# Performance work log

Hardware: AMD Instinct MI355X
Metric: run time of the kernel (lower is better)

Reference implementation:

```python
import jax, jax.numpy as jnp
import numpy as np

B, T, V, C, H, HS, L, DFF = 8192, 8, 65, 512, 8, 64, 6, 2048
LN_EPS = 1e-5


def _layernorm(x, g, b):
    mu = jnp.mean(x, axis=-1, keepdims=True)
    var = jnp.mean(jnp.square(x - mu), axis=-1, keepdims=True)
    return (x - mu) * jax.lax.rsqrt(var + LN_EPS) * g + b


def setup_inputs() -> dict:
    key = jax.random.key(0)
    ks = jax.random.split(key, 16)
    s = 0.02
    inp = {
        "idx": jax.random.randint(ks[0], (B, T), 0, V),
        "tok_table": jax.random.normal(ks[1], (V, C), jnp.float32) * s,
        "pos_table": jax.random.normal(ks[2], (T, C), jnp.float32) * s,
        "wq": jax.random.normal(ks[3], (L, H, C, HS), jnp.float32) * s,
        "wk": jax.random.normal(ks[4], (L, H, C, HS), jnp.float32) * s,
        "wv": jax.random.normal(ks[5], (L, H, C, HS), jnp.float32) * s,
        "proj_w": jax.random.normal(ks[6], (L, C, C), jnp.float32) * s,
        "proj_b": jnp.zeros((L, C), jnp.float32),
        "w1": jax.random.normal(ks[7], (L, C, DFF), jnp.float32) * s,
        "b1": jnp.zeros((L, DFF), jnp.float32),
        "w2": jax.random.normal(ks[8], (L, DFF, C), jnp.float32) * s,
        "b2": jnp.zeros((L, C), jnp.float32),
        "ln1_g": jnp.ones((L, C), jnp.float32),
        "ln1_b": jnp.zeros((L, C), jnp.float32),
        "ln2_g": jnp.ones((L, C), jnp.float32),
        "ln2_b": jnp.zeros((L, C), jnp.float32),
        "lm_w": jax.random.normal(ks[9], (C, V), jnp.float32) * s,
        "lm_b": jnp.zeros((V,), jnp.float32),
    }
    return inp


def reference(idx, tok_table, pos_table, wq, wk, wv, proj_w, proj_b,
              w1, b1, w2, b2, ln1_g, ln1_b, ln2_g, ln2_b, lm_w, lm_b):
    idx = idx[:, -T:]
    x = tok_table[idx] + pos_table[None, :T, :]  # [B,T,C]
    mask = jnp.tril(jnp.ones((T, T), bool))
    scale = C ** (-0.5)  # NOTE: original scales by n_embed, not head_size
    for l in range(L):
        q = jnp.einsum('btc,hcd->bhtd', x, wq[l])
        k = jnp.einsum('btc,hcd->bhtd', x, wk[l])
        v = jnp.einsum('btc,hcd->bhtd', x, wv[l])
        att = jnp.einsum('bhtd,bhsd->bhts', q, k) * scale
        att = jnp.where(mask, att, -jnp.inf)
        att = jax.nn.softmax(att, axis=-1)
        o = jnp.einsum('bhts,bhsd->bhtd', att, v)
        o = o.transpose(0, 2, 1, 3).reshape(x.shape[0], T, C)  # concat heads
        o = o @ proj_w[l] + proj_b[l]
        x = _layernorm(x + o, ln1_g[l], ln1_b[l])  # post-norm
        h = jax.nn.relu(x @ w1[l] + b1[l]) @ w2[l] + b2[l]
        x = _layernorm(x + h, ln2_g[l], ln2_b[l])
    logits = x @ lm_w + lm_b  # [B,T,V]
    return logits
```

## Files before the change

kernel.cpp:

```cpp
#include <hip/hip_runtime.h>
#include <hip/hip_bf16.h>
#include <math.h>

#define NTOK  65536
#define CDIM  512
#define NHEAD 8
#define HSZ   64
#define NLAYER 6
#define DFF   2048
#define VOCAB 65

typedef unsigned short u16;
typedef __attribute__((ext_vector_type(8))) __bf16 bf16x8;
typedef __attribute__((ext_vector_type(4))) float f32x4;
typedef __attribute__((ext_vector_type(8))) unsigned short ushort8;

__device__ __forceinline__ float b2f(u16 u) {
    union { unsigned int i; float f; } x; x.i = ((unsigned int)u) << 16; return x.f;
}
__device__ __forceinline__ u16 f2b(float f) {
    union { float f; unsigned int i; } x; x.f = f;
    unsigned int r = x.i + 0x7fffu + ((x.i >> 16) & 1u);
    return (u16)(r >> 16);
}

__device__ __forceinline__ void async16(const u16* g, u16* l) {
    __builtin_amdgcn_global_load_lds(
        (const __attribute__((address_space(1))) void*)g,
        (__attribute__((address_space(3))) void*)l, 16, 0, 0);
}

template<int JB, int IB>
__device__ __forceinline__ void mfma_quad(f32x4 (&acc)[4][8],
                                          const bf16x8 (&af)[4][2],
                                          const bf16x8 (&bf)[4][2])
{
#pragma unroll
    for (int kk = 0; kk < 2; kk++)
#pragma unroll
        for (int j = 0; j < 2; j++)
#pragma unroll
            for (int i = 0; i < 4; i++)
                acc[JB + j][IB + i] = __builtin_amdgcn_mfma_f32_16x16x32_bf16(
                    bf[JB + j][kk], af[i][kk], acc[JB + j][IB + i], 0, 0, 0);
}

template<int EPI>
__global__ __launch_bounds__(512, 2)
void gemm256(const u16* __restrict__ A, const u16* __restrict__ Bt,
             void* Cout, const float* __restrict__ bias,
             const u16* res, int K, int lda, int N, int Nout)
{
    extern __shared__ __attribute__((aligned(16))) u16 lds[];
    const int tid = threadIdx.x;

    const int Nx = gridDim.x;
    const int id = blockIdx.y * Nx + blockIdx.x;
    const int xcd = id & 7;
    const int j0 = id >> 3;
    const int mt = xcd + 8 * (j0 / Nx);
    const int nt = j0 - (j0 / Nx) * Nx;
    const int m0 = mt * 256, n0 = nt * 256;

    const int lane = tid & 63, wvv = tid >> 6;
    const int wvm = wvv >> 2, wvn = wvv & 3;
    const int r16 = lane & 15, quad = lane >> 4;
    const int gk0 = quad ^ (r16 & 7);
    const int g0x8 = gk0 * 8, g1x8 = (gk0 ^ 4) * 8;
    const int arow = wvm * 128 + r16;
    const int brow = wvn * 64 + r16;

    const int srow = tid >> 3;
    const int sg = (tid & 7) ^ (srow & 7);
    const u16* pA = A + (size_t)(m0 + srow) * lda + sg * 8;
    const u16* pB = Bt + (size_t)(n0 + srow) * K + sg * 8;
    u16* const ldst = lds + tid * 8;
    const size_t ldaq = (size_t)64 * lda, ldah = (size_t)128 * lda;
    const size_t kq = (size_t)64 * K, kh = (size_t)128 * K;

    const int nk = K >> 6;

    f32x4 acc[4][8] = {};
    bf16x8 af[4][2], bf[4][2];

#define STAGE_A(c, kt, h) do { \
    async16(pA + ((h) ? ldah : 0) + (size_t)((kt) * 64),        ldst + (c) * 32768 + (h) * 8192); \
    async16(pA + ((h) ? ldah : 0) + ldaq + (size_t)((kt) * 64), ldst + (c) * 32768 + (h) * 8192 + 4096); } while (0)
#define STAGE_B(c, kt, h) do { \
    async16(pB + ((h) ? kh : 0) + (size_t)((kt) * 64),          ldst + (c) * 32768 + 16384 + (h) * 8192); \
    async16(pB + ((h) ? kh : 0) + kq + (size_t)((kt) * 64),     ldst + (c) * 32768 + 16384 + (h) * 8192 + 4096); } while (0)
#define LD_A4(IB0) do { _Pragma("unroll") \
    for (int i = 0; i < 4; i++) { \
        const int ro = cb + (arow + ((IB0) + i) * 16) * 64; \
        af[i][0] = *(const bf16x8*)(const void*)&lds[ro + g0x8]; \
        af[i][1] = *(const bf16x8*)(const void*)&lds[ro + g1x8]; \
    } } while (0)
#define LD_B2(JB0) do { _Pragma("unroll") \
    for (int j = 0; j < 2; j++) { \
        const int ro = cb + 16384 + (brow + ((JB0) + j) * 16) * 64; \
        bf[(JB0) + j][0] = *(const bf16x8*)(const void*)&lds[ro + g0x8]; \
        bf[(JB0) + j][1] = *(const bf16x8*)(const void*)&lds[ro + g1x8]; \
    } } while (0)
#define LGKM0() do { asm volatile("s_waitcnt lgkmcnt(0)" ::: "memory"); \
                     __builtin_amdgcn_sched_barrier(0); } while (0)

    STAGE_A(0, 0, 0); STAGE_A(0, 0, 1);
    STAGE_B(0, 0, 0); STAGE_B(0, 0, 1);
    if (nk > 1) {
        STAGE_B(1, 1, 0); STAGE_B(1, 1, 1);
        asm volatile("s_waitcnt vmcnt(4)" ::: "memory");
    } else {
        asm volatile("s_waitcnt vmcnt(0)" ::: "memory");
    }
    __builtin_amdgcn_s_barrier();

    for (int t = 0; t < nk; ++t) {
        const int c = t & 1;
        const int cb = c * 32768;

        LD_A4(0);
        LD_B2(0);
        if (t + 1 < nk) STAGE_A(c ^ 1, t + 1, 0);
        __builtin_amdgcn_s_barrier();
        LGKM0();
        __builtin_amdgcn_s_setprio(1);
        mfma_quad<0, 0>(acc, af, bf);
        __builtin_amdgcn_s_setprio(0);
        __builtin_amdgcn_s_barrier();

        LD_B2(2);
        if (t + 1 < nk) STAGE_A(c ^ 1, t + 1, 1);
        __builtin_amdgcn_s_barrier();
        LGKM0();
        __builtin_amdgcn_s_setprio(1);
        mfma_quad<2, 0>(acc, af, bf);
        __builtin_amdgcn_s_setprio(0);
        __builtin_amdgcn_s_barrier();

        LD_A4(4);
        if (t + 2 < nk) STAGE_B(c, t + 2, 0);
        __builtin_amdgcn_s_barrier();
        LGKM0();
        __builtin_amdgcn_s_setprio(1);
        mfma_quad<0, 4>(acc, af, bf);
        __builtin_amdgcn_s_setprio(0);
        __builtin_amdgcn_s_barrier();

        if (t + 2 < nk) {
            STAGE_B(c, t + 2, 1);
            asm volatile("s_waitcnt vmcnt(4)" ::: "memory");
        } else {
            asm volatile("s_waitcnt vmcnt(0)" ::: "memory");
        }
        __builtin_amdgcn_s_barrier();
        __builtin_amdgcn_s_setprio(1);
        mfma_quad<2, 4>(acc, af, bf);
        __builtin_amdgcn_s_setprio(0);
        __builtin_amdgcn_s_barrier();
    }
#undef STAGE_A
#undef STAGE_B
#undef LD_A4
#undef LD_B2
#undef LGKM0

#pragma unroll
    for (int i = 0; i < 8; i++) {
        const int row = m0 + wvm * 128 + i * 16 + r16;
#pragma unroll
        for (int j = 0; j < 4; j++) {
            const int colb = n0 + wvn * 64 + j * 16 + quad * 4;
            float v[4];
#pragma unroll
            for (int r = 0; r < 4; r++) v[r] = acc[j][i][r];
            if (EPI == 1 || EPI == 2) {
                const f32x4 b4 = *(const f32x4*)(const void*)&bias[colb];
#pragma unroll
                for (int r = 0; r < 4; r++) v[r] += b4[r];
            }
            if (EPI == 1) {
                const uint2 rv = *(const uint2*)(const void*)&res[(size_t)row * N + colb];
                v[0] += b2f((u16)(rv.x & 0xffffu));
                v[1] += b2f((u16)(rv.x >> 16));
                v[2] += b2f((u16)(rv.y & 0xffffu));
                v[3] += b2f((u16)(rv.y >> 16));
            }
            if (EPI == 2) {
#pragma unroll
                for (int r = 0; r < 4; r++) v[r] = fmaxf(v[r], 0.f);
            }
            uint2 o;
            o.x = (unsigned)f2b(v[0]) | ((unsigned)f2b(v[1]) << 16);
            o.y = (unsigned)f2b(v[2]) | ((unsigned)f2b(v[3]) << 16);
            *(uint2*)(void*)&((u16*)Cout)[(size_t)row * N + colb] = o;
        }
    }
}

template<int EPI>
__global__ __launch_bounds__(512)
void gemm_bt(const u16* __restrict__ A, const u16* __restrict__ Bt,
             void* __restrict__ Cout, const float* __restrict__ bias,
             const u16* __restrict__ res, int K, int lda, int N, int Nout)
{
    __shared__ u16 lA[2 * 256 * 32];
    __shared__ u16 lB[2 * 128 * 32];
    const int tid  = threadIdx.x;

    const int Nx = gridDim.x;
    const int id = blockIdx.y * Nx + blockIdx.x;
    const int xcd = id & 7;
    const int j0  = id >> 3;
    const int mt  = xcd + 8 * (j0 / Nx);
    const int nt  = j0 - (j0 / Nx) * Nx;
    const int m0  = mt * 256;
    const int n0  = nt * 128;

    const int lane = tid & 63;
    const int wv   = tid >> 6;
    const int wr   = (wv >> 1) * 64;
    const int wc   = (wv & 1) * 64;
    const int r16  = lane & 15;
    const int quad = lane >> 4;

    f32x4 acc[4][4] = {};

    const int srow = tid >> 2, skseg = (tid & 3) * 8;
    const u16* pA  = A  + (size_t)(m0 + srow) * lda + skseg;
    const u16* pA2 = pA + (size_t)128 * lda;
    const u16* pB  = Bt + (size_t)(n0 + srow) * K + skseg;
    u16* lAt = &lA[(size_t)tid * 8];
    u16* lBt = &lB[(size_t)tid * 8];

    for (int k0 = 0; k0 < K; k0 += 64) {
        async16(pA  + k0,      lAt);
        async16(pA2 + k0,      lAt + 4096);
        async16(pA  + k0 + 32, lAt + 8192);
        async16(pA2 + k0 + 32, lAt + 12288);
        async16(pB  + k0,      lBt);
        async16(pB  + k0 + 32, lBt + 4096);
        __syncthreads();

#pragma unroll
        for (int s = 0; s < 2; s++) {
            const u16* bA = &lA[s * 8192];
            const u16* bB = &lB[s * 4096];
            bf16x8 af[4], bfr[4];
#pragma unroll
            for (int i = 0; i < 4; i++)
                af[i] = *(const bf16x8*)(const void*)&bA[(wr + i * 16 + r16) * 32 + quad * 8];
#pragma unroll
            for (int j = 0; j < 4; j++)
                bfr[j] = *(const bf16x8*)(const void*)&bB[(wc + j * 16 + r16) * 32 + quad * 8];
#pragma unroll
            for (int j = 0; j < 4; j++)
#pragma unroll
                for (int i = 0; i < 4; i++)
                    acc[j][i] = __builtin_amdgcn_mfma_f32_16x16x32_bf16(bfr[j], af[i], acc[j][i], 0, 0, 0);
        }
        __syncthreads();
    }

#pragma unroll
    for (int i = 0; i < 4; i++) {
        const int row = m0 + wr + i * 16 + r16;
#pragma unroll
        for (int j = 0; j < 4; j++) {
            const int colb = n0 + wc + j * 16 + quad * 4;
            float v[4];
#pragma unroll
            for (int r = 0; r < 4; r++) v[r] = acc[j][i][r];
            if (EPI == 3) {
#pragma unroll
                for (int r = 0; r < 4; r++) {
                    const int col = colb + r;
                    if (col < Nout)
                        ((float*)Cout)[(size_t)row * Nout + col] = v[r] + bias[col];
                }
            } else {
                uint2 o;
                o.x = (unsigned)f2b(v[0]) | ((unsigned)f2b(v[1]) << 16);
                o.y = (unsigned)f2b(v[2]) | ((unsigned)f2b(v[3]) << 16);
                *(uint2*)(void*)&((u16*)Cout)[(size_t)row * N + colb] = o;
            }
        }
    }
}

__global__ __launch_bounds__(256)
void attn_k(u16* __restrict__ qkv)
{
    __shared__ float sq[4][8][65], sk[4][8][65], sv[4][8][65], sp[4][64];
    const int w = threadIdx.x >> 6, lane = threadIdx.x & 63;
    const int unit = blockIdx.x * 4 + w;
    const int b = unit >> 3, h = unit & 7;
    const size_t base = (size_t)b * 8 * 1536 + h * 64;
    {
        const int t = lane >> 3, d0 = (lane & 7) * 8;
        const ushort8 q8 = *(const ushort8*)(const void*)&qkv[base + t * 1536 + d0];
        const ushort8 k8 = *(const ushort8*)(const void*)&qkv[base + t * 1536 + 512 + d0];
        const ushort8 v8 = *(const ushort8*)(const void*)&qkv[base + t * 1536 + 1024 + d0];
#pragma unroll
        for (int i = 0; i < 8; i++) {
            sq[w][t][d0 + i] = b2f(q8[i]);
            sk[w][t][d0 + i] = b2f(k8[i]);
            sv[w][t][d0 + i] = b2f(v8[i]);
        }
    }
    __syncthreads();
    const int t = lane >> 3, s = lane & 7;
    float sc = -1e30f;
    if (s <= t) {
        float d = 0.f;
#pragma unroll
        for (int c = 0; c < 64; c++) d += sq[w][t][c] * sk[w][s][c];
        sc = d * 0.04419417382415922f;
    }
    float mx = sc;
#pragma unroll
    for (int m = 1; m < 8; m <<= 1) mx = fmaxf(mx, __shfl_xor(mx, m, 8));
    float e = __expf(sc - mx);
    if (s > t) e = 0.f;
    float sum = e;
#pragma unroll
    for (int m = 1; m < 8; m <<= 1) sum += __shfl_xor(sum, m, 8);
    sp[w][lane] = e / sum;
    __syncthreads();
    {
        const int tt = lane >> 3, d0 = (lane & 7) * 8;
        float a[8] = {};
#pragma unroll
        for (int ss = 0; ss < 8; ss++) {
            const float p = sp[w][tt * 8 + ss];
#pragma unroll
            for (int i = 0; i < 8; i++) a[i] += p * sv[w][ss][d0 + i];
        }
        ushort8 o;
#pragma unroll
        for (int i = 0; i < 8; i++) o[i] = f2b(a[i]);
        *(ushort8*)(void*)&qkv[base + tt * 1536 + d0] = o;
    }
}

__global__ __launch_bounds__(256)
void ln_k(const u16* __restrict__ y, const float* __restrict__ g,
          const float* __restrict__ be, u16* __restrict__ x)
{
    const int w = threadIdx.x >> 6, lane = threadIdx.x & 63;
    const size_t tok = (size_t)blockIdx.x * 4 + w;
    const u16* row = y + tok * 512 + lane * 8;
    ushort8 raw = *(const ushort8*)(const void*)row;
    float v[8];
#pragma unroll
    for (int i = 0; i < 8; i++) v[i] = b2f(raw[i]);
    float s = 0.f;
#pragma unroll
    for (int i = 0; i < 8; i++) s += v[i];
#pragma unroll
    for (int m = 1; m < 64; m <<= 1) s += __shfl_xor(s, m, 64);
    const float mu = s * (1.f / 512.f);
    float q = 0.f;
#pragma unroll
    for (int i = 0; i < 8; i++) { float d = v[i] - mu; q += d * d; }
#pragma unroll
    for (int m = 1; m < 64; m <<= 1) q += __shfl_xor(q, m, 64);
    const float inv = rsqrtf(q * (1.f / 512.f) + 1e-5f);
    f32x4 g0  = *(const f32x4*)(const void*)&g[lane * 8];
    f32x4 g1  = *(const f32x4*)(const void*)&g[lane * 8 + 4];
    f32x4 b0  = *(const f32x4*)(const void*)&be[lane * 8];
    f32x4 b1v = *(const f32x4*)(const void*)&be[lane * 8 + 4];
    ushort8 o;
#pragma unroll
    for (int i = 0; i < 4; i++) o[i]     = f2b((v[i] - mu) * inv * g0[i] + b0[i]);
#pragma unroll
    for (int i = 0; i < 4; i++) o[i + 4] = f2b((v[i + 4] - mu) * inv * g1[i] + b1v[i]);
    *(ushort8*)(void*)&x[tok * 512 + lane * 8] = o;
}

__global__ __launch_bounds__(256)
void embed_k(const int* __restrict__ idx, const float* __restrict__ tokt,
             const float* __restrict__ pos, u16* __restrict__ xb)
{
    const int gid = blockIdx.x * 256 + threadIdx.x;
    const int tk = gid >> 6, seg = (gid & 63) * 8;
    const int t = tk & 7;
    const int ix = idx[tk];
    const f32x4 a0 = *(const f32x4*)(const void*)&tokt[(size_t)ix * 512 + seg];
    const f32x4 a1 = *(const f32x4*)(const void*)&tokt[(size_t)ix * 512 + seg + 4];
    const f32x4 p0 = *(const f32x4*)(const void*)&pos[t * 512 + seg];
    const f32x4 p1 = *(const f32x4*)(const void*)&pos[t * 512 + seg + 4];
    ushort8 o;
#pragma unroll
    for (int i = 0; i < 4; i++) o[i]     = f2b(a0[i] + p0[i]);
#pragma unroll
    for (int i = 0; i < 4; i++) o[i + 4] = f2b(a1[i] + p1[i]);
    *(ushort8*)(void*)&xb[(size_t)tk * 512 + seg] = o;
}

__global__ __launch_bounds__(256)
void conv_t2_k(const float* __restrict__ in, u16* __restrict__ out, int K, int N)
{
    __shared__ float t[32][33];
    const int tx = threadIdx.x & 31, ty4 = (threadIdx.x >> 5) * 4;
    const int n0 = blockIdx.x * 32, k0 = blockIdx.y * 32, l = blockIdx.z;
    const size_t per = (size_t)K * N;
    const float* src = in + l * per;
#pragma unroll
    for (int r = 0; r < 4; r++)
        t[ty4 + r][tx] = src[(size_t)(k0 + ty4 + r) * N + n0 + tx];
    __syncthreads();
    u16* dst = out + l * per;
#pragma unroll
    for (int r = 0; r < 4; r++)
        dst[(size_t)(n0 + ty4 + r) * K + k0 + tx] = f2b(t[tx][ty4 + r]);
}

__global__ __launch_bounds__(256)
void conv_qkv2_k(const float* __restrict__ wq, const float* __restrict__ wk,
                 const float* __restrict__ wv, u16* __restrict__ out)
{
    __shared__ float t[32][33];
    const int tx = threadIdx.x & 31, ty4 = (threadIdx.x >> 5) * 4;
    const int c0 = blockIdx.x * 32, d0 = blockIdx.y * 32;
    const int z = blockIdx.z;
    const int sel = z / 48, rem = z - sel * 48;
    const int l = rem >> 3, h = rem & 7;
    const float* src = (sel == 0) ? wq : (sel == 1) ? wk : wv;
    const float* sb = src + (((size_t)l * 8 + h) * 512) * 64;
#pragma unroll
    for (int r = 0; r < 4; r++)
        t[ty4 + r][tx] = sb[(size_t)(c0 + ty4 + r) * 64 + d0 + tx];
    __syncthreads();
    u16* dst = out + (size_t)l * 786432 + (size_t)(sel * 512 + h * 64 + d0) * 512;
#pragma unroll
    for (int r = 0; r < 4; r++)
        dst[(size_t)(ty4 + r) * 512 + c0 + tx] = f2b(t[tx][ty4 + r]);
}

__global__ __launch_bounds__(256)
void conv_lm_k(const float* __restrict__ lm_w, u16* __restrict__ out)
{
    int gid = blockIdx.x * 256 + threadIdx.x;
    int n = gid >> 9, c = gid & 511;
    out[gid] = (n < VOCAB) ? f2b(lm_w[(size_t)c * VOCAB + n]) : (u16)0;
}

extern "C" void kernel_launch(void* const* d_in, const int* in_sizes, int n_in,
                              void* d_out, int out_size, void* d_ws, size_t ws_size,
                              hipStream_t stream)
{
    const int*   idx    = (const int*)  d_in[0];
    const float* tokt   = (const float*)d_in[1];
    const float* post   = (const float*)d_in[2];
    const float* wq     = (const float*)d_in[3];
    const float* wk     = (const float*)d_in[4];
    const float* wvp    = (const float*)d_in[5];
    const float* proj_w = (const float*)d_in[6];
    const float* proj_b = (const float*)d_in[7];
    const float* w1     = (const float*)d_in[8];
    const float* b1     = (const float*)d_in[9];
    const float* w2     = (const float*)d_in[10];
    const float* b2     = (const float*)d_in[11];
    const float* ln1_g  = (const float*)d_in[12];
    const float* ln1_b  = (const float*)d_in[13];
    const float* ln2_g  = (const float*)d_in[14];
    const float* ln2_b  = (const float*)d_in[15];
    const float* lm_w   = (const float*)d_in[16];
    const float* lm_b   = (const float*)d_in[17];
    float* out = (float*)d_out;

    static int smem_set = 0;
    if (!smem_set) {
        smem_set = 1;
        hipFuncSetAttribute(reinterpret_cast<const void*>(&gemm256<0>),
                            hipFuncAttributeMaxDynamicSharedMemorySize, 131072);
        hipFuncSetAttribute(reinterpret_cast<const void*>(&gemm256<1>),
                            hipFuncAttributeMaxDynamicSharedMemorySize, 131072);
        hipFuncSetAttribute(reinterpret_cast<const void*>(&gemm256<2>),
                            hipFuncAttributeMaxDynamicSharedMemorySize, 131072);
    }

    char* ws = (char*)d_ws;
    u16* wqkvt = (u16*)(ws + 0);
    u16* wprjt = (u16*)(ws + 9437184);
    u16* ww1t  = (u16*)(ws + 12582912);
    u16* ww2t  = (u16*)(ws + 25165824);
    u16* wlmt  = (u16*)(ws + 37748736);
    u16* xb    = (u16*)(ws + 37879808);
    char* big  = ws + 104988672;

    const size_t fixed_bytes = 104988672ull;
    const size_t avail = (ws_size > fixed_bytes) ? (ws_size - fixed_bytes) : 0;
    int chunk_a = 8192, chunk_m = 8192;
    const int cands[3] = {65536, 32768, 16384};
    for (int i = 0; i < 3; i++)
        if ((size_t)cands[i] * 3072ull <= avail) { chunk_a = cands[i]; break; }
    for (int i = 0; i < 3; i++)
        if ((size_t)cands[i] * 4096ull <= avail) { chunk_m = cands[i]; break; }
    const int nca = NTOK / chunk_a, ncm = NTOK / chunk_m;
    u16* qkvc = (u16*)big;
    u16* h1c  = (u16*)big;

    conv_qkv2_k<<<dim3(16, 2, 144), 256, 0, stream>>>(wq, wk, wvp, wqkvt);
    conv_t2_k  <<<dim3(16, 16, 6), 256, 0, stream>>>(proj_w, wprjt, 512, 512);
    conv_t2_k  <<<dim3(64, 16, 6), 256, 0, stream>>>(w1, ww1t, 512, 2048);
    conv_t2_k  <<<dim3(16, 64, 6), 256, 0, stream>>>(w2, ww2t, 2048, 512);
    conv_lm_k  <<<128 * 512 / 256, 256, 0, stream>>>(lm_w, wlmt);

    embed_k<<<NTOK * 64 / 256, 256, 0, stream>>>(idx, tokt, post, xb);

    for (int l = 0; l < NLAYER; l++) {
        for (int c = 0; c < nca; c++) {
            const size_t t0 = (size_t)c * chunk_a;
            gemm256<0><<<dim3(6, chunk_a / 256), 512, 131072, stream>>>(
                xb + t0 * 512, wqkvt + (size_t)l * 786432, qkvc,
                nullptr, nullptr, 512, 512, 1536, 1536);
            attn_k<<<chunk_a / 4, 256, 0, stream>>>(qkvc);
            gemm256<1><<<dim3(2, chunk_a / 256), 512, 131072, stream>>>(
                qkvc, wprjt + (size_t)l * 262144, xb + t0 * 512,
                proj_b + l * 512, xb + t0 * 512, 512, 1536, 512, 512);
        }
        ln_k<<<NTOK / 4, 256, 0, stream>>>(xb, ln1_g + l * 512, ln1_b + l * 512, xb);
        for (int c = 0; c < ncm; c++) {
            const size_t t0 = (size_t)c * chunk_m;
            gemm256<2><<<dim3(8, chunk_m / 256), 512, 131072, stream>>>(
                xb + t0 * 512, ww1t + (size_t)l * 1048576, h1c,
                b1 + l * 2048, nullptr, 512, 512, 2048, 2048);
            gemm256<1><<<dim3(2, chunk_m / 256), 512, 131072, stream>>>(
                h1c, ww2t + (size_t)l * 1048576, xb + t0 * 512,
                b2 + l * 512, xb + t0 * 512, 2048, 2048, 512, 512);
        }
        ln_k<<<NTOK / 4, 256, 0, stream>>>(xb, ln2_g + l * 512, ln2_b + l * 512, xb);
    }

    gemm_bt<3><<<dim3(1, 256), 512, 0, stream>>>(
        xb, wlmt, out, lm_b, nullptr, 512, 512, 128, VOCAB);
}
```

Baseline: 4.115 ms.

## Make gemm256 persistent over N tiles so each block reuses its A rows

The 256-wide GEMM now launches a 1D grid of two blocks per M tile. Each block loops over several consecutive N tiles (tpb), and the B prefetch of the next N tile overlaps with the tail of the current K loop. The goal is to keep the A panel cache-hot and cut block launch and pipeline prologue costs. The trade-offs are fewer blocks, which lowers parallelism when chunks are small, and a serialized epilogue between N tiles.

```diff
diff --git a/kernel.cpp b/kernel.cpp
--- a/kernel.cpp
+++ b/kernel.cpp
@@ -49,18 +49,18 @@
 __global__ __launch_bounds__(512, 2)
 void gemm256(const u16* __restrict__ A, const u16* __restrict__ Bt,
              void* Cout, const float* __restrict__ bias,
-             const u16* res, int K, int lda, int N, int Nout)
+             const u16* res, int K, int lda, int N, int tpb)
 {
     extern __shared__ __attribute__((aligned(16))) u16 lds[];
     const int tid = threadIdx.x;
-
-    const int Nx = gridDim.x;
-    const int id = blockIdx.y * Nx + blockIdx.x;
-    const int xcd = id & 7;
-    const int j0 = id >> 3;
-    const int mt = xcd + 8 * (j0 / Nx);
-    const int nt = j0 - (j0 / Nx) * Nx;
-    const int m0 = mt * 256, n0 = nt * 256;
+    const int bid = blockIdx.x;
+
+    const int per_x = gridDim.x >> 4;
+    const int xcd = bid & 7, wblk = bid >> 3;
+    const int mt = xcd * per_x + (wblk >> 1);
+    const int q  = wblk & 1;
+    const int m0 = mt * 256;
+    const int nt0 = q * tpb;
 
     const int lane = tid & 63, wvv = tid >> 6;
     const int wvm = wvv >> 2, wvn = wvv & 3;
@@ -72,23 +72,24 @@
 
     const int srow = tid >> 3;
     const int sg = (tid & 7) ^ (srow & 7);
-    const u16* pA = A + (size_t)(m0 + srow) * lda + sg * 8;
-    const u16* pB = Bt + (size_t)(n0 + srow) * K + sg * 8;
+    const u16* pA  = A  + (size_t)(m0 + srow) * lda + sg * 8;
+    const u16* pB0 = Bt + (size_t)(nt0 * 256 + srow) * K + sg * 8;
     u16* const ldst = lds + tid * 8;
     const size_t ldaq = (size_t)64 * lda, ldah = (size_t)128 * lda;
     const size_t kq = (size_t)64 * K, kh = (size_t)128 * K;
+    const size_t bstride = (size_t)256 * K;
 
     const int nk = K >> 6;
 
-    f32x4 acc[4][8] = {};
+    f32x4 acc[4][8];
     bf16x8 af[4][2], bf[4][2];
 
 #define STAGE_A(c, kt, h) do { \
     async16(pA + ((h) ? ldah : 0) + (size_t)((kt) * 64),        ldst + (c) * 32768 + (h) * 8192); \
     async16(pA + ((h) ? ldah : 0) + ldaq + (size_t)((kt) * 64), ldst + (c) * 32768 + (h) * 8192 + 4096); } while (0)
-#define STAGE_B(c, kt, h) do { \
-    async16(pB + ((h) ? kh : 0) + (size_t)((kt) * 64),          ldst + (c) * 32768 + 16384 + (h) * 8192); \
-    async16(pB + ((h) ? kh : 0) + kq + (size_t)((kt) * 64),     ldst + (c) * 32768 + 16384 + (h) * 8192 + 4096); } while (0)
+#define STAGE_B(c, pb, kt, h) do { \
+    async16((pb) + ((h) ? kh : 0) + (size_t)((kt) * 64),        ldst + (c) * 32768 + 16384 + (h) * 8192); \
+    async16((pb) + ((h) ? kh : 0) + kq + (size_t)((kt) * 64),   ldst + (c) * 32768 + 16384 + (h) * 8192 + 4096); } while (0)
 #define LD_A4(IB0) do { _Pragma("unroll") \
     for (int i = 0; i < 4; i++) { \
         const int ro = cb + (arow + ((IB0) + i) * 16) * 64; \
@@ -105,96 +106,111 @@
                      __builtin_amdgcn_sched_barrier(0); } while (0)
 
     STAGE_A(0, 0, 0); STAGE_A(0, 0, 1);
-    STAGE_B(0, 0, 0); STAGE_B(0, 0, 1);
+    STAGE_B(0, pB0, 0, 0); STAGE_B(0, pB0, 0, 1);
     if (nk > 1) {
-        STAGE_B(1, 1, 0); STAGE_B(1, 1, 1);
+        STAGE_B(1, pB0, 1, 0); STAGE_B(1, pB0, 1, 1);
         asm volatile("s_waitcnt vmcnt(4)" ::: "memory");
     } else {
         asm volatile("s_waitcnt vmcnt(0)" ::: "memory");
     }
     __builtin_amdgcn_s_barrier();
 
-    for (int t = 0; t < nk; ++t) {
-        const int c = t & 1;
-        const int cb = c * 32768;
-
-        LD_A4(0);
-        LD_B2(0);
-        if (t + 1 < nk) STAGE_A(c ^ 1, t + 1, 0);
-        __builtin_amdgcn_s_barrier();
-        LGKM0();
-        __builtin_amdgcn_s_setprio(1);
-        mfma_quad<0, 0>(acc, af, bf);
-        __builtin_amdgcn_s_setprio(0);
-        __builtin_amdgcn_s_barrier();
-
-        LD_B2(2);
-        if (t + 1 < nk) STAGE_A(c ^ 1, t + 1, 1);
-        __builtin_amdgcn_s_barrier();
-        LGKM0();
-        __builtin_amdgcn_s_setprio(1);
-        mfma_quad<2, 0>(acc, af, bf);
-        __builtin_amdgcn_s_setprio(0);
-        __builtin_amdgcn_s_barrier();
-
-        LD_A4(4);
-        if (t + 2 < nk) STAGE_B(c, t + 2, 0);
-        __builtin_amdgcn_s_barrier();
-        LGKM0();
-        __builtin_amdgcn_s_setprio(1);
-        mfma_quad<0, 4>(acc, af, bf);
-        __builtin_amdgcn_s_setprio(0);
-        __builtin_amdgcn_s_barrier();
-
-        if (t + 2 < nk) {
-            STAGE_B(c, t + 2, 1);
-            asm volatile("s_waitcnt vmcnt(4)" ::: "memory");
-        } else {
-            asm volatile("s_waitcnt vmcnt(0)" ::: "memory");
-        }
-        __builtin_amdgcn_s_barrier();
-        __builtin_amdgcn_s_setprio(1);
-        mfma_quad<2, 4>(acc, af, bf);
-        __builtin_amdgcn_s_setprio(0);
-        __builtin_amdgcn_s_barrier();
+    for (int j = 0; j < tpb; ++j) {
+#pragma unroll
+        for (int jj = 0; jj < 4; jj++)
+#pragma unroll
+            for (int ii = 0; ii < 8; ii++)
+                acc[jj][ii] = (f32x4){0.f, 0.f, 0.f, 0.f};
+
+        for (int t = 0; t < nk; ++t) {
+            const int c = t & 1;
+            const int cb = c * 32768;
+            const bool haveA = !((j == tpb - 1) && (t == nk - 1));
+            const int kta = (t + 1 < nk) ? (t + 1) : 0;
+            int t2 = t + 2, j2 = j;
+            if (t2 >= nk) { t2 -= nk; j2++; }
+            const bool haveB = (j2 < tpb);
+            const u16* pB2 = pB0 + (size_t)j2 * bstride;
+
+            LD_A4(0);
+            LD_B2(0);
+            if (haveA) STAGE_A(c ^ 1, kta, 0);
+            __builtin_amdgcn_s_barrier();
+            LGKM0();
+            __builtin_amdgcn_s_setprio(1);
+            mfma_quad<0, 0>(acc, af, bf);
+            __builtin_amdgcn_s_setprio(0);
+            __builtin_amdgcn_s_barrier();
+
+            LD_B2(2);
+            if (haveA) STAGE_A(c ^ 1, kta, 1);
+            __builtin_amdgcn_s_barrier();
+            LGKM0();
+            __builtin_amdgcn_s_setprio(1);
+            mfma_quad<2, 0>(acc, af, bf);
+            __builtin_amdgcn_s_setprio(0);
+            __builtin_amdgcn_s_barrier();
+
+            LD_A4(4);
+            if (haveB) STAGE_B(c, pB2, t2, 0);
+            __builtin_amdgcn_s_barrier();
+            LGKM0();
+            __builtin_amdgcn_s_setprio(1);
+            mfma_quad<0, 4>(acc, af, bf);
+            __builtin_amdgcn_s_setprio(0);
+            __builtin_amdgcn_s_barrier();
+
+            if (haveB) {
+                STAGE_B(c, pB2, t2, 1);
+                asm volatile("s_waitcnt vmcnt(4)" ::: "memory");
+            } else {
+                asm volatile("s_waitcnt vmcnt(0)" ::: "memory");
+            }
+            __builtin_amdgcn_s_barrier();
+            __builtin_amdgcn_s_setprio(1);
+            mfma_quad<2, 4>(acc, af, bf);
+            __builtin_amdgcn_s_setprio(0);
+            __builtin_amdgcn_s_barrier();
+        }
+
+        const int n0 = (nt0 + j) * 256;
+#pragma unroll
+        for (int i = 0; i < 8; i++) {
+            const int row = m0 + wvm * 128 + i * 16 + r16;
+#pragma unroll
+            for (int jc = 0; jc < 4; jc++) {
+                const int colb = n0 + wvn * 64 + jc * 16 + quad * 4;
+                float v[4];
+#pragma unroll
+                for (int r = 0; r < 4; r++) v[r] = acc[jc][i][r];
+                if (EPI == 1 || EPI == 2) {
+                    const f32x4 b4 = *(const f32x4*)(const void*)&bias[colb];
+#pragma unroll
+                    for (int r = 0; r < 4; r++) v[r] += b4[r];
+                }
+                if (EPI == 1) {
+                    const uint2 rv = *(const uint2*)(const void*)&res[(size_t)row * N + colb];
+                    v[0] += b2f((u16)(rv.x & 0xffffu));
+                    v[1] += b2f((u16)(rv.x >> 16));
+                    v[2] += b2f((u16)(rv.y & 0xffffu));
+                    v[3] += b2f((u16)(rv.y >> 16));
+                }
+                if (EPI == 2) {
+#pragma unroll
+                    for (int r = 0; r < 4; r++) v[r] = fmaxf(v[r], 0.f);
+                }
+                uint2 o;
+                o.x = (unsigned)f2b(v[0]) | ((unsigned)f2b(v[1]) << 16);
+                o.y = (unsigned)f2b(v[2]) | ((unsigned)f2b(v[3]) << 16);
+                *(uint2*)(void*)&((u16*)Cout)[(size_t)row * N + colb] = o;
+            }
+        }
     }
 #undef STAGE_A
 #undef STAGE_B
 #undef LD_A4
 #undef LD_B2
 #undef LGKM0
-
-#pragma unroll
-    for (int i = 0; i < 8; i++) {
-        const int row = m0 + wvm * 128 + i * 16 + r16;
-#pragma unroll
-        for (int j = 0; j < 4; j++) {
-            const int colb = n0 + wvn * 64 + j * 16 + quad * 4;
-            float v[4];
-#pragma unroll
-            for (int r = 0; r < 4; r++) v[r] = acc[j][i][r];
-            if (EPI == 1 || EPI == 2) {
-                const f32x4 b4 = *(const f32x4*)(const void*)&bias[colb];
-#pragma unroll
-                for (int r = 0; r < 4; r++) v[r] += b4[r];
-            }
-            if (EPI == 1) {
-                const uint2 rv = *(const uint2*)(const void*)&res[(size_t)row * N + colb];
-                v[0] += b2f((u16)(rv.x & 0xffffu));
-                v[1] += b2f((u16)(rv.x >> 16));
-                v[2] += b2f((u16)(rv.y & 0xffffu));
-                v[3] += b2f((u16)(rv.y >> 16));
-            }
-            if (EPI == 2) {
-#pragma unroll
-                for (int r = 0; r < 4; r++) v[r] = fmaxf(v[r], 0.f);
-            }
-            uint2 o;
-            o.x = (unsigned)f2b(v[0]) | ((unsigned)f2b(v[1]) << 16);
-            o.y = (unsigned)f2b(v[2]) | ((unsigned)f2b(v[3]) << 16);
-            *(uint2*)(void*)&((u16*)Cout)[(size_t)row * N + colb] = o;
-        }
-    }
 }
 
 template<int EPI>
@@ -512,23 +528,25 @@
     for (int l = 0; l < NLAYER; l++) {
         for (int c = 0; c < nca; c++) {
             const size_t t0 = (size_t)c * chunk_a;
-            gemm256<0><<<dim3(6, chunk_a / 256), 512, 131072, stream>>>(
+            const int grid = (chunk_a / 256) * 2;
+            gemm256<0><<<dim3(grid), 512, 131072, stream>>>(
                 xb + t0 * 512, wqkvt + (size_t)l * 786432, qkvc,
-                nullptr, nullptr, 512, 512, 1536, 1536);
+                nullptr, nullptr, 512, 512, 1536, 3);
             attn_k<<<chunk_a / 4, 256, 0, stream>>>(qkvc);
-            gemm256<1><<<dim3(2, chunk_a / 256), 512, 131072, stream>>>(
+            gemm256<1><<<dim3(grid), 512, 131072, stream>>>(
                 qkvc, wprjt + (size_t)l * 262144, xb + t0 * 512,
-                proj_b + l * 512, xb + t0 * 512, 512, 1536, 512, 512);
+                proj_b + l * 512, xb + t0 * 512, 512, 1536, 512, 1);
         }
         ln_k<<<NTOK / 4, 256, 0, stream>>>(xb, ln1_g + l * 512, ln1_b + l * 512, xb);
         for (int c = 0; c < ncm; c++) {
             const size_t t0 = (size_t)c * chunk_m;
-            gemm256<2><<<dim3(8, chunk_m / 256), 512, 131072, stream>>>(
+            const int grid = (chunk_m / 256) * 2;
+            gemm256<2><<<dim3(grid), 512, 131072, stream>>>(
                 xb + t0 * 512, ww1t + (size_t)l * 1048576, h1c,
-                b1 + l * 2048, nullptr, 512, 512, 2048, 2048);
-            gemm256<1><<<dim3(2, chunk_m / 256), 512, 131072, stream>>>(
+                b1 + l * 2048, nullptr, 512, 512, 2048, 4);
+            gemm256<1><<<dim3(grid), 512, 131072, stream>>>(
                 h1c, ww2t + (size_t)l * 1048576, xb + t0 * 512,
-                b2 + l * 512, xb + t0 * 512, 2048, 2048, 512, 512);
+                b2 + l * 512, xb + t0 * 512, 2048, 2048, 512, 1);
         }
         ln_k<<<NTOK / 4, 256, 0, stream>>>(xb, ln2_g + l * 512, ln2_b + l * 512, xb);
     }
```

Measured after the change: 4.151 ms. About the same (+0.9%).
